# Optimization experiments

Measured on AMD Instinct MI355X. Metric: run time of the kernel, lower is better.

## Reference

```python
import jax, jax.numpy as jnp
import numpy as np

B, S, E, H = 2, 2048, 1024, 16
D = E // H  # d_k = n_wires = 64


def setup_inputs() -> dict:
    key = jax.random.key(0)
    ks = jax.random.split(key, 6)
    x = jax.random.normal(ks[0], (B, S, E), dtype=jnp.float32)
    scale = 0.02
    Wq = jax.random.normal(ks[1], (E, E), dtype=jnp.float32) * scale
    Wk = jax.random.normal(ks[2], (E, E), dtype=jnp.float32) * scale
    Wv = jax.random.normal(ks[3], (E, E), dtype=jnp.float32) * scale
    Wc = jax.random.normal(ks[4], (E, E), dtype=jnp.float32) * scale
    bc = jnp.zeros((E,), dtype=jnp.float32)
    return {"x": x, "Wq": Wq, "Wk": Wk, "Wv": Wv, "Wc": Wc, "bc": bc}


def _split_heads(t):
    # [B,S,E] -> [B,H,S,D]
    return t.reshape(B, S, H, D).transpose(0, 2, 1, 3)


def _quantum(t):
    # RX(theta_i) per wire + CNOT ladder + per-wire PauliZ expectation:
    # <Z_j> = prod_{i<=j} cos(theta_i)  (closed form of the circuit)
    return jnp.cumprod(jnp.cos(t), axis=-1)


def reference(x, Wq, Wk, Wv, Wc, bc):
    q = _quantum(_split_heads(x @ Wq.T))  # [B,H,S,D]
    k = _quantum(_split_heads(x @ Wk.T))
    v = _quantum(_split_heads(x @ Wv.T))
    scores = jnp.einsum('bhsd,bhtd->bhst', q, k) / jnp.sqrt(jnp.float32(D))
    attn = jax.nn.softmax(scores, axis=-1)
    out = jnp.einsum('bhst,bhtd->bhsd', attn, v)  # [B,H,S,D]
    out = out.transpose(0, 2, 1, 3).reshape(B, S, E)
    return out @ Wc.T + bc
```

## Files before the change

kernel.cpp:

```cpp
#include <hip/hip_runtime.h>
#include <hip/hip_bf16.h>

constexpr int Bc = 2, Sc = 2048, Ec = 1024, Hc = 16, Dc = 64;
constexpr int Mrows = Bc * Sc;
constexpr int Kdim  = Ec;

typedef float  floatx4 __attribute__((ext_vector_type(4)));
typedef short  shortx8 __attribute__((ext_vector_type(8)));

__device__ inline unsigned short f2bf(float f) {
    union { __hip_bfloat16 h; unsigned short u; } cv;
    cv.h = __float2bfloat16(f);
    return cv.u;
}
__device__ inline float bf2f(unsigned short u) {
    union { unsigned int i; float f; } c; c.i = ((unsigned int)u) << 16; return c.f;
}
__device__ inline float exp2_fast(float x) {
#if __has_builtin(__builtin_amdgcn_exp2f)
    return __builtin_amdgcn_exp2f(x);
#else
    return __expf(x * 0.69314718056f);
#endif
}

__device__ __forceinline__ void gll16(const void* g, void* lds) {
    __builtin_amdgcn_global_load_lds(
        (const __attribute__((address_space(1))) void*)g,
        (__attribute__((address_space(3))) void*)lds, 16, 0, 0);
}

__global__ __launch_bounds__(256) void convert_all_kernel(
    const float* __restrict__ x,  const float* __restrict__ Wq,
    const float* __restrict__ Wk, const float* __restrict__ Wv,
    const float* __restrict__ Wc,
    unsigned short* __restrict__ xb,  unsigned short* __restrict__ Wqb,
    unsigned short* __restrict__ Wkb, unsigned short* __restrict__ Wvb,
    unsigned short* __restrict__ Wcb)
{
    const long t = (long)blockIdx.x * 256 + threadIdx.x;
    const long i = t * 4;
    const float* src; unsigned short* dst; long off;
    if (i < 4194304) { src = x; dst = xb; off = i; }
    else {
        long j = i - 4194304;
        int wsel = (int)(j >> 20);
        off = j & 1048575;
        src = (wsel == 0) ? Wq : (wsel == 1) ? Wk : (wsel == 2) ? Wv : Wc;
        dst = (wsel == 0) ? Wqb : (wsel == 1) ? Wkb : (wsel == 2) ? Wvb : Wcb;
    }
    float4 v = *(const float4*)(src + off);
    unsigned short tmp[4] __attribute__((aligned(8)));
    tmp[0] = f2bf(v.x); tmp[1] = f2bf(v.y); tmp[2] = f2bf(v.z); tmp[3] = f2bf(v.w);
    *(uint2*)(dst + off) = *(uint2*)tmp;
}

__global__ __launch_bounds__(256) void proj_mfma_kernel(
    const unsigned short* __restrict__ Ab,
    const unsigned short* __restrict__ Wqb,
    const unsigned short* __restrict__ Wkb,
    const unsigned short* __restrict__ Wvb,
    unsigned short* __restrict__ oq,
    unsigned short* __restrict__ ok,
    unsigned short* __restrict__ ov)
{
    __shared__ __align__(16) char smem[33792];
    float (*Cs)[132] = (float(*)[132])smem;
    __shared__ float Sp[64][9];

    const int z = blockIdx.z;
    const unsigned short* Wb = (z == 0) ? Wqb : (z == 1) ? Wkb : Wvb;
    unsigned short* out      = (z == 0) ? oq  : (z == 1) ? ok  : ov;
    const int mode = (z == 2) ? 1 : 0;

    const int tid = threadIdx.x;
    const int lane = tid & 63;
    const int w = tid >> 6, l15 = tid & 15, quad = (tid >> 4) & 3;
    const int wq = w >> 1, wn = w & 1;
    const int m0 = blockIdx.x * 128;
    const int n0 = blockIdx.y * 128;
    const int h0 = n0 >> 6;
    const int sw = l15 & 7;

    floatx4 acc[4][4];
    #pragma unroll
    for (int ms = 0; ms < 4; ++ms)
        #pragma unroll
        for (int ns = 0; ns < 4; ++ns)
            #pragma unroll
            for (int e = 0; e < 4; ++e) acc[ms][ns][e] = 0.0f;

    for (int k0 = 0; k0 < Kdim; k0 += 64) {
        #pragma unroll
        for (int j = 0; j < 4; ++j) {
            int idx = j * 64 + lane;
            int row = 32 * w + (idx >> 3);
            int cg  = ((idx & 7) ^ (idx >> 3)) & 7;
            gll16(Ab + (size_t)(m0 + row) * Kdim + k0 + cg * 8,
                  smem + 4096 * w + 1024 * j);
            gll16(Wb + (size_t)(n0 + row) * Kdim + k0 + cg * 8,
                  smem + 16384 + 4096 * w + 1024 * j);
        }
        __syncthreads();
        #pragma unroll
        for (int ks = 0; ks < 2; ++ks) {
            shortx8 af[4], bf[4];
            #pragma unroll
            for (int ms = 0; ms < 4; ++ms)
                af[ms] = *(shortx8*)(smem + (64 * wq + 16 * ms + l15) * 128
                                     + (((4 * ks + quad) ^ sw) << 4));
            #pragma unroll
            for (int ns = 0; ns < 4; ++ns)
                bf[ns] = *(shortx8*)(smem + 16384 + (64 * wn + 16 * ns + l15) * 128
                                     + (((4 * ks + quad) ^ sw) << 4));
            #pragma unroll
            for (int ms = 0; ms < 4; ++ms)
                #pragma unroll
                for (int ns = 0; ns < 4; ++ns)
                    acc[ms][ns] = __builtin_amdgcn_mfma_f32_16x16x32_bf16(
                        af[ms], bf[ns], acc[ms][ns], 0, 0, 0);
        }
        __syncthreads();
    }

    const int b = m0 >> 11;
    const int sbase = m0 & (Sc - 1);

    for (int pass = 0; pass < 2; ++pass) {
        if (wq == pass) {
            #pragma unroll
            for (int ms = 0; ms < 4; ++ms)
                #pragma unroll
                for (int ns = 0; ns < 4; ++ns)
                    #pragma unroll
                    for (int r = 0; r < 4; ++r)
                        Cs[16 * ms + 4 * quad + r][64 * wn + 16 * ns + l15] =
                            __cosf(acc[ms][ns][r]);
        }
        __syncthreads();
        #pragma unroll
        for (int t = tid; t < 512; t += 256) {
            int row = t >> 3, seg = t & 7;
            float pr = 1.0f;
            #pragma unroll
            for (int c = 0; c < 16; ++c) pr *= Cs[row][seg * 16 + c];
            Sp[row][seg] = pr;
        }
        __syncthreads();
        if (mode == 0) {
            #pragma unroll
            for (int t = tid; t < 512; t += 256) {
                int row = t >> 3, seg = t & 7;
                float p = 1.0f;
                for (int j = (seg & 4); j < seg; ++j) p *= Sp[row][j];
                unsigned short tmp[16] __attribute__((aligned(16)));
                #pragma unroll
                for (int c = 0; c < 16; ++c) { p *= Cs[row][seg * 16 + c]; tmp[c] = f2bf(p); }
                int h = h0 + (seg >> 2);
                int s = sbase + pass * 64 + row;
                size_t base = (((size_t)b * Hc + h) * Sc + s) * Dc + (seg & 3) * 16;
                *(shortx8*)(out + base)     = *(shortx8*)&tmp[0];
                *(shortx8*)(out + base + 8) = *(shortx8*)&tmp[8];
            }
            __syncthreads();
        } else {
            #pragma unroll
            for (int t = tid; t < 512; t += 256) {
                int row = t >> 3, seg = t & 7;
                float p = 1.0f;
                for (int j = (seg & 4); j < seg; ++j) p *= Sp[row][j];
                #pragma unroll
                for (int c = 0; c < 16; ++c) { p *= Cs[row][seg * 16 + c]; Cs[row][seg * 16 + c] = p; }
            }
            __syncthreads();
            #pragma unroll
            for (int t = tid; t < 512; t += 256) {
                int col = t >> 2, chunk = t & 3;
                int h = h0 + (col >> 6), d = col & 63;
                unsigned short tmp[16] __attribute__((aligned(16)));
                #pragma unroll
                for (int j = 0; j < 16; ++j) tmp[j] = f2bf(Cs[chunk * 16 + j][col]);
                size_t base = (((size_t)b * Hc + h) * Dc + d) * Sc
                              + sbase + pass * 64 + chunk * 16;
                *(shortx8*)(out + base)     = *(shortx8*)&tmp[0];
                *(shortx8*)(out + base + 8) = *(shortx8*)&tmp[8];
            }
            __syncthreads();
        }
    }
}

__global__ __launch_bounds__(256) void attn_mfma_kernel(
    const unsigned short* __restrict__ qg,
    const unsigned short* __restrict__ kg,
    const unsigned short* __restrict__ vtg,
    unsigned short* __restrict__ o1,
    unsigned short* __restrict__ o2,
    float* __restrict__ lpart)
{
    __shared__ __align__(16) char smem[34816];
    unsigned short (*Pq)[72] = (unsigned short(*)[72])(smem + 16384);

    const int tid  = threadIdx.x;
    const int lane = tid & 63;
    const int w    = tid >> 6;
    const int l15  = tid & 15;
    const int quad = (tid >> 4) & 3;
    const int qb   = blockIdx.x;
    const int half = blockIdx.y;
    const int bh   = blockIdx.z;
    const int sw   = l15 & 7;

    const unsigned short* qp = qg  + (size_t)bh * Sc * Dc;
    const unsigned short* kp = kg  + (size_t)bh * Sc * Dc;
    const unsigned short* vp = vtg + (size_t)bh * Dc * Sc;

    int qrow[2];
    shortx8 qf[2][2];
    #pragma unroll
    for (int qs = 0; qs < 2; ++qs) {
        qrow[qs] = qb * 128 + 32 * w + 16 * qs + l15;
        qf[qs][0] = *(const shortx8*)(qp + (size_t)qrow[qs] * Dc + 8 * quad);
        qf[qs][1] = *(const shortx8*)(qp + (size_t)qrow[qs] * Dc + 32 + 8 * quad);
    }

    floatx4 Oacc[2][4];
    #pragma unroll
    for (int qs = 0; qs < 2; ++qs)
        #pragma unroll
        for (int mt = 0; mt < 4; ++mt)
            #pragma unroll
            for (int e = 0; e < 4; ++e) Oacc[qs][mt][e] = 0.0f;
    float lsum[2] = {0.0f, 0.0f};

    const float cexp = 0.125f * 1.442695041f;

    for (int kt = half * 16; kt < half * 16 + 16; ++kt) {
        #pragma unroll
        for (int j = 0; j < 2; ++j) {
            int idx = j * 64 + lane;
            int row = 16 * w + (idx >> 3);
            int cg  = ((idx & 7) ^ (idx >> 3)) & 7;
            gll16(kp + (size_t)(kt * 64 + row) * Dc + cg * 8,
                  smem + 2048 * w + 1024 * j);
            gll16(vp + (size_t)row * Sc + kt * 64 + cg * 8,
                  smem + 8192 + 2048 * w + 1024 * j);
        }
        __syncthreads();

        shortx8 kf[2][4], vf[2][4];
        #pragma unroll
        for (int ks = 0; ks < 2; ++ks)
            #pragma unroll
            for (int mt = 0; mt < 4; ++mt) {
                int off = (16 * mt + l15) * 128 + (((4 * ks + quad) ^ sw) << 4);
                kf[ks][mt] = *(shortx8*)(smem + off);
                vf[ks][mt] = *(shortx8*)(smem + 8192 + off);
            }

        #pragma unroll
        for (int qs = 0; qs < 2; ++qs) {
            floatx4 st[4];
            #pragma unroll
            for (int mt = 0; mt < 4; ++mt)
                #pragma unroll
                for (int e = 0; e < 4; ++e) st[mt][e] = 0.0f;
            #pragma unroll
            for (int ks = 0; ks < 2; ++ks)
                #pragma unroll
                for (int mt = 0; mt < 4; ++mt)
                    st[mt] = __builtin_amdgcn_mfma_f32_16x16x32_bf16(
                        kf[ks][mt], qf[qs][ks], st[mt], 0, 0, 0);

            float rs = 0.0f;
            #pragma unroll
            for (int mt = 0; mt < 4; ++mt) {
                float p0 = exp2_fast(st[mt][0] * cexp);
                float p1 = exp2_fast(st[mt][1] * cexp);
                float p2 = exp2_fast(st[mt][2] * cexp);
                float p3 = exp2_fast(st[mt][3] * cexp);
                rs += (p0 + p1) + (p2 + p3);
                unsigned short tmp[4] __attribute__((aligned(8)));
                tmp[0] = f2bf(p0); tmp[1] = f2bf(p1); tmp[2] = f2bf(p2); tmp[3] = f2bf(p3);
                *(uint2*)&Pq[32 * w + 16 * qs + l15][16 * mt + 4 * quad] = *(uint2*)tmp;
            }
            lsum[qs] += rs;

            #pragma unroll
            for (int ks = 0; ks < 2; ++ks) {
                shortx8 pf = *(shortx8*)&Pq[32 * w + 16 * qs + l15][32 * ks + 8 * quad];
                #pragma unroll
                for (int mt = 0; mt < 4; ++mt)
                    Oacc[qs][mt] = __builtin_amdgcn_mfma_f32_16x16x32_bf16(
                        vf[ks][mt], pf, Oacc[qs][mt], 0, 0, 0);
            }
        }
        __syncthreads();
    }

    const int b = bh >> 4, hh = bh & 15;
    unsigned short* opart = half ? o2 : o1;
    float* lp = lpart + ((size_t)half * (Bc * Hc) + bh) * Sc;
    #pragma unroll
    for (int qs = 0; qs < 2; ++qs) {
        float l = lsum[qs];
        l += __shfl_xor(l, 16, 64);
        l += __shfl_xor(l, 32, 64);
        if (quad == 0) lp[qrow[qs]] = l;
        #pragma unroll
        for (int mt = 0; mt < 4; ++mt) {
            unsigned short tmp[4] __attribute__((aligned(8)));
            #pragma unroll
            for (int r = 0; r < 4; ++r) tmp[r] = f2bf(Oacc[qs][mt][r]);
            size_t base = ((size_t)b * Sc + qrow[qs]) * Ec + hh * 64 + 16 * mt + 4 * quad;
            *(uint2*)(opart + base) = *(uint2*)tmp;
        }
    }
}

__global__ __launch_bounds__(256) void combine_kernel(
    unsigned short* __restrict__ o1,
    const unsigned short* __restrict__ o2,
    const float* __restrict__ lpart)
{
    const size_t t = (size_t)blockIdx.x * 256 + threadIdx.x;
    const size_t base = t * 8;
    const int e = (int)(base & (Ec - 1));
    const int h = e >> 6;
    const size_t bs = base >> 10;
    const int b = (int)(bs >> 11), s = (int)(bs & (Sc - 1));
    const int bh = b * Hc + h;
    const float l = lpart[(size_t)bh * Sc + s]
                  + lpart[(size_t)(Bc * Hc + bh) * Sc + s];
    const float inv = 1.0f / l;
    uint4 a = *(const uint4*)(o1 + base);
    uint4 c = *(const uint4*)(o2 + base);
    const unsigned short* ua = (const unsigned short*)&a;
    const unsigned short* uc = (const unsigned short*)&c;
    unsigned short r[8] __attribute__((aligned(16)));
    #pragma unroll
    for (int i = 0; i < 8; ++i)
        r[i] = f2bf((bf2f(ua[i]) + bf2f(uc[i])) * inv);
    *(uint4*)(o1 + base) = *(uint4*)r;
}

__global__ __launch_bounds__(256) void outproj_mfma_kernel(
    const unsigned short* __restrict__ Ab,
    const unsigned short* __restrict__ Wb,
    const float* __restrict__ bias,
    float* __restrict__ out)
{
    __shared__ __align__(16) char smem[24576];

    const int tid = threadIdx.x;
    const int lane = tid & 63;
    const int w = tid >> 6, l15 = tid & 15, quad = (tid >> 4) & 3;
    const int wq = w >> 1, wn = w & 1;
    const int m0 = blockIdx.x * 64;
    const int n0 = blockIdx.y * 128;
    const int sw = l15 & 7;

    floatx4 acc[2][4];
    #pragma unroll
    for (int ms = 0; ms < 2; ++ms)
        #pragma unroll
        for (int ns = 0; ns < 4; ++ns)
            #pragma unroll
            for (int e = 0; e < 4; ++e) acc[ms][ns][e] = 0.0f;

    for (int k0 = 0; k0 < Kdim; k0 += 64) {
        #pragma unroll
        for (int j = 0; j < 2; ++j) {
            int idx = j * 64 + lane;
            int row = 16 * w + (idx >> 3);
            int cg  = ((idx & 7) ^ (idx >> 3)) & 7;
            gll16(Ab + (size_t)(m0 + row) * Kdim + k0 + cg * 8,
                  smem + 2048 * w + 1024 * j);
        }
        #pragma unroll
        for (int j = 0; j < 4; ++j) {
            int idx = j * 64 + lane;
            int row = 32 * w + (idx >> 3);
            int cg  = ((idx & 7) ^ (idx >> 3)) & 7;
            gll16(Wb + (size_t)(n0 + row) * Kdim + k0 + cg * 8,
                  smem + 8192 + 4096 * w + 1024 * j);
        }
        __syncthreads();
        #pragma unroll
        for (int ks = 0; ks < 2; ++ks) {
            shortx8 af[2], bf[4];
            #pragma unroll
            for (int ms = 0; ms < 2; ++ms)
                af[ms] = *(shortx8*)(smem + (32 * wq + 16 * ms + l15) * 128
                                     + (((4 * ks + quad) ^ sw) << 4));
            #pragma unroll
            for (int ns = 0; ns < 4; ++ns)
                bf[ns] = *(shortx8*)(smem + 8192 + (64 * wn + 16 * ns + l15) * 128
                                     + (((4 * ks + quad) ^ sw) << 4));
            #pragma unroll
            for (int ms = 0; ms < 2; ++ms)
                #pragma unroll
                for (int ns = 0; ns < 4; ++ns)
                    acc[ms][ns] = __builtin_amdgcn_mfma_f32_16x16x32_bf16(
                        af[ms], bf[ns], acc[ms][ns], 0, 0, 0);
        }
        __syncthreads();
    }

    #pragma unroll
    for (int ns = 0; ns < 4; ++ns) {
        const float bv = bias[n0 + 64 * wn + 16 * ns + l15];
        #pragma unroll
        for (int ms = 0; ms < 2; ++ms)
            #pragma unroll
            for (int r = 0; r < 4; ++r) {
                int m = m0 + 32 * wq + 16 * ms + 4 * quad + r;
                out[(size_t)m * Kdim + n0 + 64 * wn + 16 * ns + l15] = acc[ms][ns][r] + bv;
            }
    }
}

extern "C" void kernel_launch(void* const* d_in, const int* in_sizes, int n_in,
                              void* d_out, int out_size, void* d_ws, size_t ws_size,
                              hipStream_t stream) {
    const float* x  = (const float*)d_in[0];
    const float* Wq = (const float*)d_in[1];
    const float* Wk = (const float*)d_in[2];
    const float* Wv = (const float*)d_in[3];
    const float* Wc = (const float*)d_in[4];
    const float* bc = (const float*)d_in[5];
    float* out = (float*)d_out;

    char* p = (char*)d_ws;
    unsigned short* xb   = (unsigned short*)(p);
    unsigned short* Wqb  = (unsigned short*)(p + (8u << 20));
    unsigned short* Wkb  = (unsigned short*)(p + (10u << 20));
    unsigned short* Wvb  = (unsigned short*)(p + (12u << 20));
    unsigned short* Wcb  = (unsigned short*)(p + (14u << 20));
    unsigned short* qb_  = (unsigned short*)(p + (16u << 20));
    unsigned short* kb_  = (unsigned short*)(p + (24u << 20));
    unsigned short* vtb  = (unsigned short*)(p + (32u << 20));
    unsigned short* attb = (unsigned short*)(p + (40u << 20));
    unsigned short* o2b  = xb;
    float*          lpart = (float*)(p + (8u << 20));

    hipLaunchKernelGGL(convert_all_kernel, dim3(8192), dim3(256), 0, stream,
                       x, Wq, Wk, Wv, Wc, xb, Wqb, Wkb, Wvb, Wcb);

    hipLaunchKernelGGL(proj_mfma_kernel, dim3(Mrows / 128, Ec / 128, 3), dim3(256), 0, stream,
                       xb, Wqb, Wkb, Wvb, qb_, kb_, vtb);

    hipLaunchKernelGGL(attn_mfma_kernel, dim3(Sc / 128, 2, Bc * Hc), dim3(256), 0, stream,
                       qb_, kb_, vtb, attb, o2b, lpart);

    hipLaunchKernelGGL(combine_kernel, dim3(Mrows * Ec / (256 * 8)), dim3(256), 0, stream,
                       attb, o2b, lpart);

    hipLaunchKernelGGL(outproj_mfma_kernel, dim3(Mrows / 64, Ec / 128), dim3(256), 0, stream,
                       attb, Wcb, bc, out);
}
```

Before: 211.8 us.

## Double-buffer K/V tiles and keep P in registers via lane shuffles

The attention loop now stages K/V tiles into two alternating LDS buffers, so the next tile's global-to-LDS loads overlap compute on the current one, and it drops one barrier per iteration. The probability tile no longer round-trips through LDS. Probabilities are packed with v_cvt_pk_bf16_f32 and rearranged into MFMA operand layout with xor shuffles. This trades LDS traffic and a barrier for extra shuffle instructions and higher register pressure from holding both P fragments and V fragments.

After: 211.9 us. No clear change (+0.1%).

```diff
diff --git a/kernel.cpp b/kernel.cpp
--- a/kernel.cpp
+++ b/kernel.cpp
@@ -22,6 +22,29 @@
 #else
     return __expf(x * 0.69314718056f);
 #endif
+}
+
+__device__ __forceinline__ unsigned cvtpk_bf16(float lo, float hi) {
+    unsigned r;
+    asm("v_cvt_pk_bf16_f32 %0, %1, %2" : "=v"(r) : "v"(lo), "v"(hi));
+    return r;
+}
+
+__device__ __forceinline__ void swap32(unsigned& a, unsigned& b, int lane) {
+    unsigned a2 = __shfl_xor(a, 32, 64);
+    unsigned b2 = __shfl_xor(b, 32, 64);
+    const bool lo = (lane & 32) == 0;
+    unsigned na = lo ? a : b2;
+    unsigned nb = lo ? a2 : b;
+    a = na; b = nb;
+}
+__device__ __forceinline__ void swap16(unsigned& a, unsigned& b, int lane) {
+    unsigned a2 = __shfl_xor(a, 16, 64);
+    unsigned b2 = __shfl_xor(b, 16, 64);
+    const bool lo = (lane & 16) == 0;
+    unsigned na = lo ? a : b2;
+    unsigned nb = lo ? a2 : b;
+    a = na; b = nb;
 }
 
 __device__ __forceinline__ void gll16(const void* g, void* lds) {
@@ -198,8 +221,7 @@
     unsigned short* __restrict__ o2,
     float* __restrict__ lpart)
 {
-    __shared__ __align__(16) char smem[34816];
-    unsigned short (*Pq)[72] = (unsigned short(*)[72])(smem + 16384);
+    __shared__ __align__(16) char smem[32768];
 
     const int tid  = threadIdx.x;
     const int lane = tid & 63;
@@ -235,29 +257,38 @@
 
     const float cexp = 0.125f * 1.442695041f;
 
-    for (int kt = half * 16; kt < half * 16 + 16; ++kt) {
+    auto stage = [&](int kt, int buf) {
         #pragma unroll
         for (int j = 0; j < 2; ++j) {
             int idx = j * 64 + lane;
             int row = 16 * w + (idx >> 3);
             int cg  = ((idx & 7) ^ (idx >> 3)) & 7;
             gll16(kp + (size_t)(kt * 64 + row) * Dc + cg * 8,
-                  smem + 2048 * w + 1024 * j);
+                  smem + (buf << 14) + 2048 * w + 1024 * j);
             gll16(vp + (size_t)row * Sc + kt * 64 + cg * 8,
-                  smem + 8192 + 2048 * w + 1024 * j);
-        }
-        __syncthreads();
-
-        shortx8 kf[2][4], vf[2][4];
+                  smem + (buf << 14) + 8192 + 2048 * w + 1024 * j);
+        }
+    };
+
+    int cur = 0;
+    stage(half * 16, 0);
+
+    for (int it = 0; it < 16; ++it) {
+        const int kt = half * 16 + it;
+        __syncthreads();
+        if (it < 15) stage(kt + 1, cur ^ 1);
+
+        const char* kb = smem + (cur << 14);
+
+        shortx8 kf[2][4];
         #pragma unroll
         for (int ks = 0; ks < 2; ++ks)
             #pragma unroll
-            for (int mt = 0; mt < 4; ++mt) {
-                int off = (16 * mt + l15) * 128 + (((4 * ks + quad) ^ sw) << 4);
-                kf[ks][mt] = *(shortx8*)(smem + off);
-                vf[ks][mt] = *(shortx8*)(smem + 8192 + off);
-            }
-
+            for (int mt = 0; mt < 4; ++mt)
+                kf[ks][mt] = *(shortx8*)(kb + (16 * mt + l15) * 128
+                                         + (((4 * ks + quad) ^ sw) << 4));
+
+        unsigned pu[2][4], pw[2][4];
         #pragma unroll
         for (int qs = 0; qs < 2; ++qs) {
             floatx4 st[4];
@@ -280,22 +311,37 @@
                 float p2 = exp2_fast(st[mt][2] * cexp);
                 float p3 = exp2_fast(st[mt][3] * cexp);
                 rs += (p0 + p1) + (p2 + p3);
-                unsigned short tmp[4] __attribute__((aligned(8)));
-                tmp[0] = f2bf(p0); tmp[1] = f2bf(p1); tmp[2] = f2bf(p2); tmp[3] = f2bf(p3);
-                *(uint2*)&Pq[32 * w + 16 * qs + l15][16 * mt + 4 * quad] = *(uint2*)tmp;
+                pu[qs][mt] = cvtpk_bf16(p0, p1);
+                pw[qs][mt] = cvtpk_bf16(p2, p3);
             }
             lsum[qs] += rs;
-
+        }
+
+        shortx8 vf[2][4];
+        #pragma unroll
+        for (int ks = 0; ks < 2; ++ks)
+            #pragma unroll
+            for (int mt = 0; mt < 4; ++mt)
+                vf[ks][mt] = *(shortx8*)(kb + 8192 + (16 * mt + l15) * 128
+                                         + (((4 * ks + quad) ^ sw) << 4));
+
+        #pragma unroll
+        for (int qs = 0; qs < 2; ++qs)
             #pragma unroll
             for (int ks = 0; ks < 2; ++ks) {
-                shortx8 pf = *(shortx8*)&Pq[32 * w + 16 * qs + l15][32 * ks + 8 * quad];
+                unsigned a = pu[qs][2 * ks], b = pu[qs][2 * ks + 1];
+                unsigned c = pw[qs][2 * ks], d = pw[qs][2 * ks + 1];
+                swap32(a, b, lane); swap16(a, b, lane);
+                swap32(c, d, lane); swap16(c, d, lane);
+                union { unsigned x[4]; shortx8 s; } pf;
+                pf.x[0] = a; pf.x[1] = c; pf.x[2] = b; pf.x[3] = d;
                 #pragma unroll
                 for (int mt = 0; mt < 4; ++mt)
                     Oacc[qs][mt] = __builtin_amdgcn_mfma_f32_16x16x32_bf16(
-                        vf[ks][mt], pf, Oacc[qs][mt], 0, 0, 0);
+                        vf[ks][mt], pf.s, Oacc[qs][mt], 0, 0, 0);
             }
-        }
-        __syncthreads();
+
+        cur ^= 1;
     }
 
     const int b = bh >> 4, hh = bh & 15;
```
